# Performance work log

Hardware: AMD Instinct MI355X
Metric: run time of the kernel (lower is better)

Reference implementation:

```python
import jax, jax.numpy as jnp
import numpy as np

OUT = 7          # roi_size
SCALE = 0.0625   # spatial_scale = 1/16


def roi_pool(x, rois, roi_indices):
    """Faithful RoIPooling2D: scale coords, truncate to int (floor for >=0),
    crop [y1:y2+1, x1:x2+1] and AdaptiveMaxPool2d to (OUT, OUT).
    torch adaptive pool bin i over size h: [floor(i*h/OUT), ceil((i+1)*h/OUT)).
    Implemented as separable masked max (rows then cols), vectorized over ROIs.
    """
    H, W = x.shape[2], x.shape[3]
    coords = jnp.floor(rois * SCALE).astype(jnp.int32)  # (y1,x1,y2,x2), all >= 0
    y1, x1, y2, x2 = coords[:, 0], coords[:, 1], coords[:, 2], coords[:, 3]
    h = y2 - y1 + 1  # [R] region heights (>=1)
    w = x2 - x1 + 1  # [R] region widths  (>=1)
    feat = x[roi_indices]  # [R, C, H, W] irregular gather
    NEG = jnp.finfo(x.dtype).min
    ys = jnp.arange(H)
    xs = jnp.arange(W)
    # --- row pooling: [R, C, OUT, W] ---
    rows = []
    for i in range(OUT):
        s = y1 + (i * h) // OUT                      # floor(i*h/OUT)
        e = y1 + ((i + 1) * h + OUT - 1) // OUT      # ceil((i+1)*h/OUT)
        m = (ys[None, :] >= s[:, None]) & (ys[None, :] < e[:, None])  # [R, H]
        rows.append(jnp.max(jnp.where(m[:, None, :, None], feat, NEG), axis=2))
    rowp = jnp.stack(rows, axis=2)  # [R, C, OUT, W]
    # --- col pooling: [R, C, OUT, OUT] ---
    cols = []
    for j in range(OUT):
        s = x1 + (j * w) // OUT
        e = x1 + ((j + 1) * w + OUT - 1) // OUT
        m = (xs[None, :] >= s[:, None]) & (xs[None, :] < e[:, None])  # [R, W]
        cols.append(jnp.max(jnp.where(m[:, None, None, :], rowp, NEG), axis=3))
    return jnp.stack(cols, axis=3)  # [R, C, OUT, OUT]


def setup_inputs() -> dict:
    key = jax.random.key(0)
    ks = jax.random.split(key, 9)
    N, C, H, W = 1, 512, 37, 50   # VGG16 conv5_3 map for a 592x800 image
    R = 128                        # sampled ROIs per image
    NC = 21                        # VOC classes + background
    x = jax.random.normal(ks[0], (N, C, H, W), dtype=jnp.float32)
    # rois = (y1, x1, y2, x2) in image coords, strictly inside the image
    yy = jnp.sort(jax.random.uniform(ks[1], (R, 2), dtype=jnp.float32) * (H * 16 - 1), axis=1)
    xx = jnp.sort(jax.random.uniform(ks[2], (R, 2), dtype=jnp.float32) * (W * 16 - 1), axis=1)
    rois = jnp.stack([yy[:, 0], xx[:, 0], yy[:, 1], xx[:, 1]], axis=1)
    roi_indices = jnp.zeros((R,), dtype=jnp.int32)
    d_in = C * OUT * OUT  # 25088
    w_fc6 = jax.random.normal(ks[3], (d_in, 4096), jnp.float32) * 0.01
    b_fc6 = jnp.zeros((4096,), jnp.float32)
    w_fc7 = jax.random.normal(ks[4], (4096, 4096), jnp.float32) * 0.01
    b_fc7 = jnp.zeros((4096,), jnp.float32)
    w_cls = jax.random.normal(ks[5], (4096, NC * 4), jnp.float32) * 0.001
    b_cls = jnp.zeros((NC * 4,), jnp.float32)
    w_score = jax.random.normal(ks[6], (4096, NC), jnp.float32) * 0.01
    b_score = jnp.zeros((NC,), jnp.float32)
    return {"x": x, "rois": rois, "roi_indices": roi_indices,
            "w_fc6": w_fc6, "b_fc6": b_fc6, "w_fc7": w_fc7, "b_fc7": b_fc7,
            "w_cls": w_cls, "b_cls": b_cls, "w_score": w_score, "b_score": b_score}


def reference(x, rois, roi_indices, w_fc6, b_fc6, w_fc7, b_fc7, w_cls, b_cls, w_score, b_score):
    pool = roi_pool(x, rois, roi_indices)          # [R, 512, 7, 7]
    flat = pool.reshape(pool.shape[0], -1)          # [R, 25088]
    fc6 = jax.nn.relu(flat @ w_fc6 + b_fc6)         # [R, 4096]
    fc7 = jax.nn.relu(fc6 @ w_fc7 + b_fc7)          # [R, 4096]
    roi_cls_locs = fc7 @ w_cls + b_cls              # [R, 84]
    roi_scores = fc7 @ w_score + b_score            # [R, 21]
    return (roi_cls_locs, roi_scores)
```

## Files before the change

### kernel.cpp

```cpp
#include <hip/hip_runtime.h>
#include <hip/hip_bf16.h>


typedef short short8 __attribute__((ext_vector_type(8)));
typedef float f32x4 __attribute__((ext_vector_type(4)));
typedef int   int4v __attribute__((ext_vector_type(4)));

#define TN 64
#define SK 34

static __device__ inline unsigned bfround(float f) {
    return __builtin_bit_cast(unsigned, f) + 0x8000u;
}
static __device__ inline short f2bf(float f) { return (short)(bfround(f) >> 16); }

__global__ void pool_kernel(const float* __restrict__ x, const float* __restrict__ rois,
                            const int* __restrict__ ridx, short* __restrict__ A) {
    const int r = blockIdx.x;
    const int y1 = (int)floorf(rois[r * 4 + 0] * 0.0625f);
    const int x1 = (int)floorf(rois[r * 4 + 1] * 0.0625f);
    const int y2 = (int)floorf(rois[r * 4 + 2] * 0.0625f);
    const int x2 = (int)floorf(rois[r * 4 + 3] * 0.0625f);
    const int h = y2 - y1 + 1, w = x2 - x1 + 1;
    const float* feat = x + (size_t)ridx[r] * (512 * 37 * 50);
    for (int t = blockIdx.y * 256 + threadIdx.x; t < 25088; t += 2048) {
        const int c = t / 49, b = t % 49, i = b / 7, j = b % 7;
        const int ys = y1 + (i * h) / 7, ye = y1 + ((i + 1) * h + 6) / 7;
        const int xs = x1 + (j * w) / 7, xe = x1 + ((j + 1) * w + 6) / 7;
        const float* f = feat + c * 1850;
        float m = -1e30f;
        for (int yy = ys; yy < ye; yy++)
            for (int xx = xs; xx < xe; xx++)
                m = fmaxf(m, f[yy * 50 + xx]);
        A[(size_t)r * 25088 + t] = f2bf(m);
    }
}

__global__ void build_whd(const float* __restrict__ wc, const float* __restrict__ wsc,
                          float* __restrict__ whd) {
    const int idx = blockIdx.x * 256 + threadIdx.x;
    const int k = idx >> 7, n = idx & 127;
    float v = 0.f;
    if (n < 84) v = wc[k * 84 + n];
    else if (n < 105) v = wsc[k * 21 + (n - 84)];
    whd[idx] = v;
}

__global__ __launch_bounds__(256, 4)
void gemm128(const short* __restrict__ A, const float* __restrict__ W,
             float* __restrict__ part, int K, int N, int kchunk) {
    __shared__ short lds[2][TN * SK];

    const int tid = threadIdx.x;
    const int lane = tid & 63, wave = tid >> 6;
    const int l15 = lane & 15, quad = lane >> 4;
    const int n_base = blockIdx.x * TN;
    const int kb = blockIdx.y * kchunk;
    const int m0 = wave * 32;
    const int steps = kchunk >> 5;

    const int kp = tid >> 4;
    const int nb = (tid & 15) * 4;
    const float* gW = W + (size_t)(kb + 2 * kp) * N + n_base + nb;
    const short* gA = A + (size_t)(m0 + l15) * K + kb + quad * 8;

    f32x4 acc[2][4] = {};
    f32x4 wset[2][2];
    short8 aset[2][2];

    auto wload = [&](int s, int c) {
        const float* p = gW + (size_t)s * 32 * N;
        wset[c][0] = *(const f32x4*)p;
        wset[c][1] = *(const f32x4*)(p + N);
    };
    auto aload = [&](int s, int c) {
        const short* p = gA + (size_t)s * 32;
        aset[c][0] = *(const short8*)p;
        aset[c][1] = *(const short8*)(p + (size_t)16 * K);
    };
    auto stage = [&](int c, int buf) {
        unsigned* dst = (unsigned*)&lds[buf][0];
#pragma unroll
        for (int i = 0; i < 4; i++) {
            unsigned lo = bfround(wset[c][0][i]) >> 16;
            unsigned hi = bfround(wset[c][1][i]) & 0xffff0000u;
            dst[((nb + i) * SK + 2 * kp) >> 1] = lo | hi;
        }
    };

    wload(0, 0); wload(1, 1);
    aload(0, 0); aload(1, 1);
    stage(0, 0);

    for (int s = 0; s < steps; s += 2) {
#pragma unroll
        for (int half = 0; half < 2; half++) {
            const int ss = s + half;
            const int C = half;
            if (ss + 2 < steps) wload(ss + 2, C);
            __syncthreads();
            const short* buf = &lds[C][0];
#pragma unroll
            for (int fn = 0; fn < 4; fn++) {
                const int* src = (const int*)(buf + (fn * 16 + l15) * SK + quad * 8);
                int4v t;
                t[0] = src[0]; t[1] = src[1]; t[2] = src[2]; t[3] = src[3];
                short8 bfr = __builtin_bit_cast(short8, t);
                acc[0][fn] = __builtin_amdgcn_mfma_f32_16x16x32_bf16(aset[C][0], bfr, acc[0][fn], 0, 0, 0);
                acc[1][fn] = __builtin_amdgcn_mfma_f32_16x16x32_bf16(aset[C][1], bfr, acc[1][fn], 0, 0, 0);
            }
            if (ss + 2 < steps) aload(ss + 2, C);
            if (ss + 1 < steps) stage(C ^ 1, C ^ 1);
        }
    }

    float* out = part + (size_t)blockIdx.y * 128 * N;
#pragma unroll
    for (int t = 0; t < 2; t++)
#pragma unroll
        for (int fn = 0; fn < 4; fn++)
#pragma unroll
            for (int r = 0; r < 4; r++) {
                const int row = m0 + 16 * t + quad * 4 + r;
                const int col = n_base + fn * 16 + l15;
                out[(size_t)row * N + col] = acc[t][fn][r];
            }
}

__global__ void reduce_fc(const float* __restrict__ part, const float* __restrict__ bias,
                          short* __restrict__ out, int N, int nslabs) {
    const int idx = blockIdx.x * 256 + threadIdx.x;
    const int n = idx % N;
    float s = bias[n];
    for (int sl = 0; sl < nslabs; sl++) s += part[(size_t)sl * 128 * N + idx];
    s = fmaxf(s, 0.f);
    out[idx] = f2bf(s);
}

__global__ void reduce_heads(const float* __restrict__ part, const float* __restrict__ bc,
                             const float* __restrict__ bsc, float* __restrict__ out) {
    const int idx = blockIdx.x * 256 + threadIdx.x;
    if (idx >= 128 * 105) return;
    const int m = idx / 105, n = idx % 105;
    float s = 0.f;
    for (int sl = 0; sl < 32; sl++) s += part[sl * (128 * 128) + m * 128 + n];
    if (n < 84) out[m * 84 + n] = s + bc[n];
    else out[128 * 84 + m * 21 + (n - 84)] = s + bsc[n - 84];
}

extern "C" void kernel_launch(void* const* d_in, const int* in_sizes, int n_in,
                              void* d_out, int out_size, void* d_ws, size_t ws_size,
                              hipStream_t stream) {
    const float* x    = (const float*)d_in[0];
    const float* rois = (const float*)d_in[1];
    const int*   ridx = (const int*)d_in[2];
    const float* w6   = (const float*)d_in[3];
    const float* b6   = (const float*)d_in[4];
    const float* w7   = (const float*)d_in[5];
    const float* b7   = (const float*)d_in[6];
    const float* wc   = (const float*)d_in[7];
    const float* bc   = (const float*)d_in[8];
    const float* wsc  = (const float*)d_in[9];
    const float* bsc  = (const float*)d_in[10];
    float* out = (float*)d_out;

    char* base = (char*)d_ws;
    short* Apool = (short*)base;
    float* whd   = (float*)(base + 6422528);
    short* fc6b  = (short*)(base + 8519680);
    short* fc7b  = (short*)(base + 9568256);
    float* slabs = (float*)(base + 10616832);
    const size_t slab_base = 10616832;
    const size_t slab_bytes = (size_t)128 * 4096 * 4;

    int ns6 = 8, ks6 = 3136;
    if (ws_size >= slab_base + 28 * slab_bytes)      { ns6 = 28; ks6 = 896; }
    else if (ws_size >= slab_base + 14 * slab_bytes) { ns6 = 14; ks6 = 1792; }
    int ns7 = 8, ks7 = 512;
    if (ws_size >= slab_base + 16 * slab_bytes)      { ns7 = 16; ks7 = 256; }

    pool_kernel<<<dim3(128, 8), 256, 0, stream>>>(x, rois, ridx, Apool);
    build_whd<<<2048, 256, 0, stream>>>(wc, wsc, whd);

    gemm128<<<dim3(64, ns6), 256, 0, stream>>>(Apool, w6, slabs, 25088, 4096, ks6);
    reduce_fc<<<2048, 256, 0, stream>>>(slabs, b6, fc6b, 4096, ns6);

    gemm128<<<dim3(64, ns7), 256, 0, stream>>>(fc6b, w7, slabs, 4096, 4096, ks7);
    reduce_fc<<<2048, 256, 0, stream>>>(slabs, b7, fc7b, 4096, ns7);

    gemm128<<<dim3(2, 32), 256, 0, stream>>>(fc7b, whd, slabs, 4096, 128, 128);
    reduce_heads<<<53, 256, 0, stream>>>(slabs, bc, bsc, out);
}
```

Before: 725.8 us.

## Widen GEMM tile to 128 columns and stage A operand through shared memory

```diff
diff --git a/kernel.cpp b/kernel.cpp
--- a/kernel.cpp
+++ b/kernel.cpp
@@ -6,8 +6,9 @@
 typedef float f32x4 __attribute__((ext_vector_type(4)));
 typedef int   int4v __attribute__((ext_vector_type(4)));
 
-#define TN 64
+#define TN 128
 #define SK 34
+#define SKA 40
 
 static __device__ inline unsigned bfround(float f) {
     return __builtin_bit_cast(unsigned, f) + 0x8000u;
@@ -46,27 +47,31 @@
     whd[idx] = v;
 }
 
-__global__ __launch_bounds__(256, 4)
+__global__ __launch_bounds__(512, 4)
 void gemm128(const short* __restrict__ A, const float* __restrict__ W,
              float* __restrict__ part, int K, int N, int kchunk) {
-    __shared__ short lds[2][TN * SK];
+    __shared__ short ldsW[2][TN * SK];
+    __shared__ short ldsA[2][128 * SKA];
 
     const int tid = threadIdx.x;
     const int lane = tid & 63, wave = tid >> 6;
     const int l15 = lane & 15, quad = lane >> 4;
+    const int wm = wave & 3;
+    const int wn = wave >> 2;
     const int n_base = blockIdx.x * TN;
     const int kb = blockIdx.y * kchunk;
-    const int m0 = wave * 32;
     const int steps = kchunk >> 5;
 
-    const int kp = tid >> 4;
-    const int nb = (tid & 15) * 4;
+    const int kp = tid >> 5;
+    const int nb = (tid & 31) * 4;
     const float* gW = W + (size_t)(kb + 2 * kp) * N + n_base + nb;
-    const short* gA = A + (size_t)(m0 + l15) * K + kb + quad * 8;
+    const int am = tid >> 2;
+    const int kq = tid & 3;
+    const short* gA = A + (size_t)am * K + kb + kq * 8;
 
     f32x4 acc[2][4] = {};
     f32x4 wset[2][2];
-    short8 aset[2][2];
+    short8 aglob[2];
 
     auto wload = [&](int s, int c) {
         const float* p = gW + (size_t)s * 32 * N;
@@ -74,18 +79,17 @@
         wset[c][1] = *(const f32x4*)(p + N);
     };
     auto aload = [&](int s, int c) {
-        const short* p = gA + (size_t)s * 32;
-        aset[c][0] = *(const short8*)p;
-        aset[c][1] = *(const short8*)(p + (size_t)16 * K);
+        aglob[c] = *(const short8*)(gA + (size_t)s * 32);
     };
     auto stage = [&](int c, int buf) {
-        unsigned* dst = (unsigned*)&lds[buf][0];
+        unsigned* dst = (unsigned*)&ldsW[buf][0];
 #pragma unroll
         for (int i = 0; i < 4; i++) {
             unsigned lo = bfround(wset[c][0][i]) >> 16;
             unsigned hi = bfround(wset[c][1][i]) & 0xffff0000u;
-            dst[((nb + i) * SK + 2 * kp) >> 1] = lo | hi;
+            dst[(nb + i) * (SK / 2) + kp] = lo | hi;
         }
+        *(short8*)(&ldsA[buf][am * SKA + kq * 8]) = aglob[c];
     };
 
     wload(0, 0); wload(1, 1);
@@ -99,15 +103,18 @@
             const int C = half;
             if (ss + 2 < steps) wload(ss + 2, C);
             __syncthreads();
-            const short* buf = &lds[C][0];
+            const short* bufA = &ldsA[C][0];
+            short8 afr0 = *(const short8*)(bufA + (wm * 32 + l15) * SKA + quad * 8);
+            short8 afr1 = *(const short8*)(bufA + (wm * 32 + 16 + l15) * SKA + quad * 8);
+            const short* bufW = &ldsW[C][0];
 #pragma unroll
             for (int fn = 0; fn < 4; fn++) {
-                const int* src = (const int*)(buf + (fn * 16 + l15) * SK + quad * 8);
+                const int* src = (const int*)(bufW + (wn * 64 + fn * 16 + l15) * SK + quad * 8);
                 int4v t;
                 t[0] = src[0]; t[1] = src[1]; t[2] = src[2]; t[3] = src[3];
                 short8 bfr = __builtin_bit_cast(short8, t);
-                acc[0][fn] = __builtin_amdgcn_mfma_f32_16x16x32_bf16(aset[C][0], bfr, acc[0][fn], 0, 0, 0);
-                acc[1][fn] = __builtin_amdgcn_mfma_f32_16x16x32_bf16(aset[C][1], bfr, acc[1][fn], 0, 0, 0);
+                acc[0][fn] = __builtin_amdgcn_mfma_f32_16x16x32_bf16(afr0, bfr, acc[0][fn], 0, 0, 0);
+                acc[1][fn] = __builtin_amdgcn_mfma_f32_16x16x32_bf16(afr1, bfr, acc[1][fn], 0, 0, 0);
             }
             if (ss + 2 < steps) aload(ss + 2, C);
             if (ss + 1 < steps) stage(C ^ 1, C ^ 1);
@@ -121,8 +128,8 @@
         for (int fn = 0; fn < 4; fn++)
 #pragma unroll
             for (int r = 0; r < 4; r++) {
-                const int row = m0 + 16 * t + quad * 4 + r;
-                const int col = n_base + fn * 16 + l15;
+                const int row = wm * 32 + 16 * t + quad * 4 + r;
+                const int col = n_base + wn * 64 + fn * 16 + l15;
                 out[(size_t)row * N + col] = acc[t][fn][r];
             }
 }
@@ -182,12 +189,12 @@
     pool_kernel<<<dim3(128, 8), 256, 0, stream>>>(x, rois, ridx, Apool);
     build_whd<<<2048, 256, 0, stream>>>(wc, wsc, whd);
 
-    gemm128<<<dim3(64, ns6), 256, 0, stream>>>(Apool, w6, slabs, 25088, 4096, ks6);
+    gemm128<<<dim3(32, ns6), 512, 0, stream>>>(Apool, w6, slabs, 25088, 4096, ks6);
     reduce_fc<<<2048, 256, 0, stream>>>(slabs, b6, fc6b, 4096, ns6);
 
-    gemm128<<<dim3(64, ns7), 256, 0, stream>>>(fc6b, w7, slabs, 4096, 4096, ks7);
+    gemm128<<<dim3(32, ns7), 512, 0, stream>>>(fc6b, w7, slabs, 4096, 4096, ks7);
     reduce_fc<<<2048, 256, 0, stream>>>(slabs, b7, fc7b, 4096, ns7);
 
-    gemm128<<<dim3(2, 32), 256, 0, stream>>>(fc7b, whd, slabs, 4096, 128, 128);
+    gemm128<<<dim3(1, 32), 512, 0, stream>>>(fc7b, whd, slabs, 4096, 128, 128);
     reduce_heads<<<53, 256, 0, stream>>>(slabs, bc, bsc, out);
 }
```

Result: faster. 699.2 us (-3.7%).
